# Optimization experiments

Hardware: AMD Instinct MI355X
Metric: run time of the kernel (lower is better)

## Reference

```python
import jax, jax.numpy as jnp
import numpy as np

N_IMG = 8
IMG_H = IMG_W = 1024
STRIDES = (4, 8, 16, 32, 64)
FEAT = tuple(IMG_H // s for s in STRIDES)
RATIOS = (0.5, 1.0, 2.0)
A = len(RATIOS)
PRE_NMS = 1000
POST_NMS = 1000
NMS_THRESH = 0.7
SCORE_THRESH = 0.0
MIN_SIZE = 1e-3
BBOX_CLIP = float(np.log(1000.0 / 16.0))  # torchvision bbox_xform_clip
NPL = tuple(f * f * A for f in FEAT)      # anchors per level


def _make_anchors():
    levels = []
    for stride, f in zip(STRIDES, FEAT):
        size = stride * 8.0
        base = []
        for r in RATIOS:
            w = size * np.sqrt(1.0 / r)
            h = size * np.sqrt(r)
            base.append([-w / 2, -h / 2, w / 2, h / 2])
        base = np.asarray(base, np.float32)              # [A,4]
        coords = np.arange(f, dtype=np.float32) * stride
        sy, sx = np.meshgrid(coords, coords, indexing="ij")
        shifts = np.stack([sx, sy, sx, sy], -1).reshape(-1, 1, 4)  # y-major, matches [H,W,A] flatten
        levels.append((shifts + base[None]).reshape(-1, 4))
    return np.concatenate(levels, 0).astype(np.float32)


def setup_inputs() -> dict:
    key = jax.random.key(0)
    ks = jax.random.split(key, 10)
    inp = {}
    for i, f in enumerate(FEAT):
        inp[f"obj_l{i}"] = jax.random.normal(ks[i], (N_IMG, A, f, f), jnp.float32)
        inp[f"delta_l{i}"] = jax.random.normal(ks[5 + i], (N_IMG, A * 4, f, f), jnp.float32) * 0.2
    inp["anchors"] = jnp.asarray(_make_anchors())
    return inp


def _flatten_level(obj, delta):
    # permute_and_flatten: [N,A,H,W] -> [N,H*W*A] ; [N,A*4,H,W] -> [N,H*W*A,4]
    n, a, h, w = obj.shape
    o = jnp.transpose(obj, (0, 2, 3, 1)).reshape(n, -1)
    d = jnp.transpose(delta.reshape(n, a, 4, h, w), (0, 3, 4, 1, 2)).reshape(n, -1, 4)
    return o, d


def _decode(deltas, anchors):
    # BoxCoder(weights=(1,1,1,1)).decode
    w = anchors[:, 2] - anchors[:, 0]
    h = anchors[:, 3] - anchors[:, 1]
    cx = anchors[:, 0] + 0.5 * w
    cy = anchors[:, 1] + 0.5 * h
    dx, dy = deltas[..., 0], deltas[..., 1]
    dw = jnp.minimum(deltas[..., 2], BBOX_CLIP)
    dh = jnp.minimum(deltas[..., 3], BBOX_CLIP)
    pcx = dx * w + cx
    pcy = dy * h + cy
    pw = jnp.exp(dw) * w
    ph = jnp.exp(dh) * h
    return jnp.stack([pcx - 0.5 * pw, pcy - 0.5 * ph, pcx + 0.5 * pw, pcy + 0.5 * ph], -1)


def _nms_image(boxes, scores, lvl):
    # clip_boxes_to_image
    x1 = jnp.clip(boxes[:, 0], 0.0, IMG_W)
    y1 = jnp.clip(boxes[:, 1], 0.0, IMG_H)
    x2 = jnp.clip(boxes[:, 2], 0.0, IMG_W)
    y2 = jnp.clip(boxes[:, 3], 0.0, IMG_H)
    boxes = jnp.stack([x1, y1, x2, y2], -1)
    # remove_small_boxes + score_thresh, as a mask (fixed shapes)
    valid = (x2 - x1 >= MIN_SIZE) & (y2 - y1 >= MIN_SIZE) & (scores >= SCORE_THRESH)
    s = jnp.where(valid, scores, -1.0)
    order = jnp.argsort(-s)
    boxes, s, valid, lvl = boxes[order], s[order], valid[order], lvl[order]
    # batched_nms: offset boxes per level so cross-level IoU is 0
    ob = boxes + (lvl.astype(boxes.dtype) * (max(IMG_H, IMG_W) + 1.0))[:, None]
    ob = jax.lax.stop_gradient(ob)  # keep decisions are non-differentiable
    area = (ob[:, 2] - ob[:, 0]) * (ob[:, 3] - ob[:, 1])
    lt = jnp.maximum(ob[:, None, :2], ob[None, :, :2])
    rb = jnp.minimum(ob[:, None, 2:], ob[None, :, 2:])
    wh = jnp.maximum(rb - lt, 0.0)
    inter = wh[..., 0] * wh[..., 1]
    iou = inter / (area[:, None] + area[None, :] - inter + 1e-9)  # [K,K]
    k = boxes.shape[0]
    jidx = jnp.arange(k)

    def body(i, keep):
        sup = keep[i] & (iou[i] > NMS_THRESH) & (jidx > i)
        return keep & ~sup

    keep = jax.lax.fori_loop(0, k, body, valid)
    # compact kept boxes (score-sorted) into fixed [POST_NMS] output, zero-padded
    rank = jnp.cumsum(keep) - 1
    tgt = jnp.where(keep & (rank < POST_NMS), rank, POST_NMS)
    out_b = jnp.zeros((POST_NMS + 1, 4), boxes.dtype).at[tgt].set(boxes)[:POST_NMS]
    out_s = jnp.zeros((POST_NMS + 1,), s.dtype).at[tgt].set(jnp.where(keep, s, 0.0))[:POST_NMS]
    return out_b, out_s


def _forward(objs, deltas, anchors):
    flat = [_flatten_level(o, d) for o, d in zip(objs, deltas)]
    obj = jnp.concatenate([f[0] for f in flat], 1)       # [N, K_total]
    dl = jnp.concatenate([f[1] for f in flat], 1)        # [N, K_total, 4]
    proposals = _decode(dl, anchors)                     # [N, K_total, 4]
    lvl_full = jnp.concatenate([jnp.full((n,), i, jnp.int32) for i, n in enumerate(NPL)])
    # per-level top-k on objectness logits
    idxs, off = [], 0
    for n in NPL:
        kk = min(PRE_NMS, n)
        _, ti = jax.lax.top_k(obj[:, off:off + n], kk)
        idxs.append(ti + off)
        off += n
    top_idx = jnp.concatenate(idxs, 1)                   # [N, K_sel]
    scores = jax.nn.sigmoid(jnp.take_along_axis(obj, top_idx, 1))
    prop = jnp.take_along_axis(proposals, top_idx[..., None], 1)
    lvl = lvl_full[top_idx]
    boxes_out, _ = jax.lax.map(lambda t: _nms_image(*t), (prop, scores, lvl))
    return boxes_out                                     # [N, POST_NMS, 4]


def reference(obj_l0, obj_l1, obj_l2, obj_l3, obj_l4, delta_l0, delta_l1, delta_l2, delta_l3, delta_l4, anchors):
    return _forward([obj_l0, obj_l1, obj_l2, obj_l3, obj_l4],
                    [delta_l0, delta_l1, delta_l2, delta_l3, delta_l4], anchors)
```

## Files before the change

### kernel.cpp

```cpp
#include <hip/hip_runtime.h>
#include <cstdint>

#define K_SEL 4768
#define CAND_CAP 16384
#define NBIN 4096
#define BUFCAP 512
#define TPAD 9216

struct P5 { const float* p[5]; };

__device__ __forceinline__ unsigned fsortkey(float f) {
  unsigned b = __float_as_uint(f);
  return (b & 0x80000000u) ? ~b : (b | 0x80000000u);
}

__global__ __launch_bounds__(256) void k_hist(P5 obj, unsigned* phist) {
  int p = blockIdx.y; int img = p / 5, lvl = p % 5;
  int f = 256 >> lvl; int n = 3 * f * f;
  __shared__ unsigned lh[NBIN];
  for (int b = threadIdx.x; b < NBIN; b += 256) lh[b] = 0;
  __syncthreads();
  const float4* src4 = (const float4*)(obj.p[lvl] + (size_t)img * n);
  int n4 = n >> 2;
  int chunk = (n4 + gridDim.x - 1) / gridDim.x;
  int e0 = blockIdx.x * chunk, e1 = min(n4, e0 + chunk);
  for (int e = e0 + threadIdx.x; e < e1; e += 256) {
    float4 v = src4[e];
    atomicAdd(&lh[fsortkey(v.x) >> 20], 1u);
    atomicAdd(&lh[fsortkey(v.y) >> 20], 1u);
    atomicAdd(&lh[fsortkey(v.z) >> 20], 1u);
    atomicAdd(&lh[fsortkey(v.w) >> 20], 1u);
  }
  __syncthreads();
  unsigned* dst = phist + ((size_t)(p * 8 + blockIdx.x)) * NBIN;
  for (int b = threadIdx.x; b < NBIN; b += 256) dst[b] = lh[b];
}

__global__ __launch_bounds__(256) void k_thresh(const unsigned* phist, int* Bthr, unsigned* cnt) {
  int p = blockIdx.x; int lvl = p % 5;
  unsigned kk = (lvl == 4) ? 768u : 1000u;
  __shared__ unsigned hsum[NBIN];
  __shared__ unsigned csum[256];
  int c = threadIdx.x;
  unsigned tot[16];
#pragma unroll
  for (int k = 0; k < 16; ++k) tot[k] = 0;
  for (int g = 0; g < 8; ++g) {
    const unsigned* hp = phist + ((size_t)(p * 8 + g)) * NBIN + c * 16;
#pragma unroll
    for (int k = 0; k < 16; ++k) tot[k] += hp[k];
  }
  unsigned s = 0;
#pragma unroll
  for (int k = 0; k < 16; ++k) { hsum[c * 16 + k] = tot[k]; s += tot[k]; }
  csum[c] = s;
  __syncthreads();
  if (c == 0) {
    unsigned acc = 0; int B = 0;
    for (int cc = 255; cc >= 0; --cc) {
      if (acc + csum[cc] >= kk) {
        for (int b = 15; b >= 0; --b) {
          acc += hsum[cc * 16 + b];
          if (acc >= kk) { B = cc * 16 + b; break; }
        }
        break;
      }
      acc += csum[cc];
    }
    Bthr[p] = B;
    cnt[p] = 0;
  }
}

__global__ __launch_bounds__(256) void k_gather(P5 obj, const int* Bthr, unsigned* cnt,
                                                unsigned long long* ck) {
  int p = blockIdx.y; int img = p / 5, lvl = p % 5;
  int f = 256 >> lvl; int hw = f * f; int n = 3 * hw;
  int B = Bthr[p];
  int shift = 2 * (8 - lvl);
  const float4* src4 = (const float4*)(obj.p[lvl] + (size_t)img * n);
  int n4 = n >> 2;
  unsigned long long* dst = ck + (size_t)p * CAND_CAP;
  int tid = threadIdx.x;
  int lane = tid & 63, wv = tid >> 6;
  __shared__ unsigned long long buf[4][BUFCAP];
  __shared__ unsigned wTot[4];
  __shared__ unsigned blkBase;
  unsigned wc = 0;
  for (int e = blockIdx.x * 256 + tid; e < n4; e += gridDim.x * 256) {
    float4 v = src4[e];
    float vv[4] = {v.x, v.y, v.z, v.w};
#pragma unroll
    for (int j = 0; j < 4; ++j) {
      unsigned sv = fsortkey(vv[j]);
      bool pass = (int)(sv >> 20) >= B;
      unsigned long long m = __ballot(pass);
      if (m) {
        if (pass) {
          unsigned pos = wc + (unsigned)__popcll(m & ((1ULL << lane) - 1ULL));
          int ee = e * 4 + j;
          int a = ee >> shift;
          int r = ee & (hw - 1);
          unsigned kidx = (unsigned)(r * 3 + a);
          unsigned long long key = ((unsigned long long)sv << 32) | (0xFFFFFFFFu - kidx);
          if (pos < BUFCAP) buf[wv][pos] = key;
          else {
            unsigned gp = atomicAdd(&cnt[p], 1u);
            if (gp < CAND_CAP) dst[gp] = key;
          }
        }
        wc += (unsigned)__popcll(m);
      }
    }
  }
  if (lane == 0) wTot[wv] = min(wc, (unsigned)BUFCAP);
  __syncthreads();
  if (tid == 0) {
    unsigned tot = wTot[0] + wTot[1] + wTot[2] + wTot[3];
    blkBase = tot ? atomicAdd(&cnt[p], tot) : 0u;
  }
  __syncthreads();
  unsigned myOff = blkBase;
  for (int x = 0; x < wv; ++x) myOff += wTot[x];
  unsigned wn = wTot[wv];
  for (unsigned j = lane; j < wn; j += 64) {
    unsigned gp = myOff + j;
    if (gp < CAND_CAP) dst[gp] = buf[wv][j];
  }
}

__global__ __launch_bounds__(256) void k_select(const unsigned* cnt, const unsigned long long* ck,
                                                unsigned* selSV, unsigned* selIdx) {
  int p = blockIdx.y; int img = p / 5, lvl = p % 5;
  int Cc = min((int)cnt[p], CAND_CAP);
  if (blockIdx.x * 256 >= Cc) return;
  int kk = (lvl == 4) ? 768 : 1000;
  int soff = lvl * 1000;
  const unsigned long long* keys = ck + (size_t)p * CAND_CAP;
  __shared__ unsigned long long sk[4096];
  int stage = min(Cc, 4096);
  for (int j = threadIdx.x; j < stage; j += 256) sk[j] = keys[j];
  __syncthreads();
  int c = blockIdx.x * 256 + threadIdx.x;
  if (c >= Cc) return;
  unsigned long long kc = keys[c];
  int rank = 0;
#pragma unroll 8
  for (int j = 0; j < stage; ++j) rank += (sk[j] > kc) ? 1 : 0;
  for (int j = stage; j < Cc; ++j) rank += (keys[j] > kc) ? 1 : 0;
  if (rank < kk) {
    int slot = img * K_SEL + soff + rank;
    selSV[slot]  = (unsigned)(kc >> 32);
    selIdx[slot] = 0xFFFFFFFFu - (unsigned)kc;
  }
}

__global__ __launch_bounds__(256) void k_decode(P5 del, const float* anchors,
                                                const unsigned* selSV, const unsigned* selIdx,
                                                float* boxP, unsigned long long* keyP) {
  int i = blockIdx.x * 256 + threadIdx.x;
  if (i >= K_SEL) return;
  int img = blockIdx.y;
  int lvl = (i < 4000) ? (i / 1000) : 4;
  int f = 256 >> lvl, hw = f * f;
  const int aoffA[5] = {0, 196608, 245760, 258048, 261120};
  int slot = img * K_SEL + i;
  unsigned k = selIdx[slot];
  unsigned sv = selSV[slot];
  int a = (int)(k % 3u); int r = (int)(k / 3u);
  int y = r >> (8 - lvl); int x = r & (f - 1);
  const float* dp = del.p[lvl] + (size_t)(img * 12 + a * 4) * hw + (size_t)y * f + x;
  float d0 = dp[0], d1 = dp[hw], d2 = dp[2 * hw], d3 = dp[3 * hw];
  const float* ar = anchors + (size_t)(aoffA[lvl] + (int)k) * 4;
  float a0 = ar[0], a1 = ar[1], a2 = ar[2], a3 = ar[3];
  float w = __fsub_rn(a2, a0), h = __fsub_rn(a3, a1);
  float cx = __fadd_rn(a0, __fmul_rn(0.5f, w));
  float cy = __fadd_rn(a1, __fmul_rn(0.5f, h));
  const float CLIP = 4.135166556742356f;
  float dw = fminf(d2, CLIP), dh = fminf(d3, CLIP);
  float pcx = __fadd_rn(__fmul_rn(d0, w), cx);
  float pcy = __fadd_rn(__fmul_rn(d1, h), cy);
  float pw = __fmul_rn(expf(dw), w);
  float ph = __fmul_rn(expf(dh), h);
  float x1 = __fsub_rn(pcx, __fmul_rn(0.5f, pw));
  float y1 = __fsub_rn(pcy, __fmul_rn(0.5f, ph));
  float x2 = __fadd_rn(pcx, __fmul_rn(0.5f, pw));
  float y2 = __fadd_rn(pcy, __fmul_rn(0.5f, ph));
  float x1c = fminf(fmaxf(x1, 0.0f), 1024.0f);
  float y1c = fminf(fmaxf(y1, 0.0f), 1024.0f);
  float x2c = fminf(fmaxf(x2, 0.0f), 1024.0f);
  float y2c = fminf(fmaxf(y2, 0.0f), 1024.0f);
  bool valid = (__fsub_rn(x2c, x1c) >= 1e-3f) && (__fsub_rn(y2c, y1c) >= 1e-3f);
  float* bp = boxP + (size_t)slot * 4;
  bp[0] = x1c; bp[1] = y1c; bp[2] = x2c; bp[3] = y2c;
  unsigned low = 0xFFFFFFFFu - (unsigned)i;
  keyP[slot] = valid ? (((unsigned long long)sv << 32) | low) : (unsigned long long)low;
}

__device__ __forceinline__ bool iou_gt(float rx1, float ry1, float rx2, float ry2, float rar,
                                       float cx1, float cy1, float cx2, float cy2, float car) {
  float ltx = fmaxf(rx1, cx1), lty = fmaxf(ry1, cy1);
  float rbx = fminf(rx2, cx2), rby = fminf(ry2, cy2);
  float wx = fmaxf(__fsub_rn(rbx, ltx), 0.0f);
  float wy = fmaxf(__fsub_rn(rby, lty), 0.0f);
  float inter = __fmul_rn(wx, wy);
  float denom = __fadd_rn(__fsub_rn(__fadd_rn(rar, car), inter), 1e-9f);
  return __fdiv_rn(inter, denom) > 0.7f;
}

__global__ __launch_bounds__(64) void k_lvlmask(const float* boxP, unsigned long long* T) {
  int img = blockIdx.y;
  int q = blockIdx.x;
  int lvl, q2;
  if (q < 544) { lvl = q / 136; q2 = q - lvl * 136; }
  else         { lvl = 4;       q2 = q - 544; }
  int kk = (lvl == 4) ? 768 : 1000;
  int nch = (kk + 63) >> 6;
  int rb = 0;
  while (q2 >= nch - rb) { q2 -= nch - rb; ++rb; }
  int cb = rb + q2;
  int t = threadIdx.x;
  float off = __fmul_rn((float)lvl, 1025.0f);
  const float4* b4 = (const float4*)boxP + (size_t)img * K_SEL + lvl * 1000;
  __shared__ float rx1s[64], ry1s[64], rx2s[64], ry2s[64], rars[64];
  int j = rb * 64 + t;
  if (j < kk) {
    float4 bb = b4[j];
    float ox1 = __fadd_rn(bb.x, off), oy1 = __fadd_rn(bb.y, off);
    float ox2 = __fadd_rn(bb.z, off), oy2 = __fadd_rn(bb.w, off);
    rx1s[t] = ox1; ry1s[t] = oy1; rx2s[t] = ox2; ry2s[t] = oy2;
    rars[t] = __fmul_rn(__fsub_rn(ox2, ox1), __fsub_rn(oy2, oy1));
  }
  __syncthreads();
  int i = cb * 64 + t;
  if (i >= kk) return;
  float4 bb = b4[i];
  float cx1 = __fadd_rn(bb.x, off), cy1 = __fadd_rn(bb.y, off);
  float cx2 = __fadd_rn(bb.z, off), cy2 = __fadd_rn(bb.w, off);
  float car = __fmul_rn(__fsub_rn(cx2, cx1), __fsub_rn(cy2, cy1));
  int jmaxR = min(64, kk - rb * 64);
  int jend = (rb == cb) ? min(t, jmaxR) : jmaxR;
  unsigned long long bits = 0;
  for (int jj = 0; jj < jend; ++jj) {
    if (iou_gt(rx1s[jj], ry1s[jj], rx2s[jj], ry2s[jj], rars[jj], cx1, cy1, cx2, cy2, car))
      bits |= (1ULL << jj);
  }
  const int Pt[16] = {0, 1, 4, 7, 12, 17, 24, 31, 40, 49, 60, 71, 84, 97, 112, 127};
  int sc = (cb + 1) | 1;
  T[(size_t)(img * 5 + lvl) * TPAD + 64 * Pt[cb] + t * sc + rb] = bits;
}

__global__ __launch_bounds__(256) void k_lvlnms(const unsigned long long* keyP,
                                                const unsigned long long* Tg_,
                                                unsigned long long* keepw) {
  int p = blockIdx.x; int img = p / 5, lvl = p % 5;
  int kk = (lvl == 4) ? 768 : 1000;
  int tw = (lvl == 4) ? 5376 : TPAD;
  int tid = threadIdx.x;
  __shared__ __align__(16) unsigned long long Ts[TPAD];
  const unsigned long long* Tg = Tg_ + (size_t)p * TPAD;
  const unsigned long long* kp = keyP + (size_t)img * K_SEL + lvl * 1000;
  unsigned vmask = 0;
  if (tid < 64) {
#pragma unroll
    for (int c = 0; c < 16; ++c) {
      int i = c * 64 + tid;
      bool v = (i < kk) && ((kp[min(i, kk - 1)] >> 32) != 0ULL);
      vmask |= v ? (1u << c) : 0u;
    }
  }
  for (int x = tid; x < (tw >> 1); x += 256)
    ((ulonglong2*)Ts)[x] = ((const ulonglong2*)Tg)[x];
  __syncthreads();
  if (tid >= 64) return;
  int t = tid;
  const int Pt[16] = {0, 1, 4, 7, 12, 17, 24, 31, 40, 49, 60, 71, 84, 97, 112, 127};
  unsigned long long kw[16];
#pragma unroll
  for (int w = 0; w < 16; ++w) kw[w] = 0ULL;
#pragma unroll
  for (int c = 0; c < 16; ++c) {
    if (c * 64 < kk) {
      int base = 64 * Pt[c] + t * ((c + 1) | 1);
      unsigned long long tv[16];
#pragma unroll
      for (int w = 0; w < 16; ++w) tv[w] = Ts[base + w];
      unsigned long long a = 0;
#pragma unroll
      for (int w = 0; w < 16; ++w) a |= tv[w] & kw[w];
      unsigned long long colT = tv[c];
      bool alive = ((vmask >> c) & 1u) && (a == 0ULL);
      unsigned long long keepm = 0ULL;
      unsigned long long actm = __ballot(alive);
      while (actm) {
        bool cank = alive && ((colT & actm) == 0ULL);
        unsigned long long newk = __ballot(cank);
        keepm |= newk;
        alive = alive && !cank && ((colT & newk) == 0ULL);
        actm = __ballot(alive);
      }
      kw[c] = keepm;
    }
  }
  if (t == 0) {
#pragma unroll
    for (int c = 0; c < 16; ++c) keepw[(size_t)p * 16 + c] = kw[c];
  }
}

__global__ __launch_bounds__(256) void k_merge(const unsigned long long* keyP, const float* boxP,
                                               const unsigned long long* keepw, float* out) {
  int p = blockIdx.x; int img = p / 5, lvl = p % 5;
  int tid = threadIdx.x;
  __shared__ unsigned long long lkey[5000];
  __shared__ int lpos[5000];
  __shared__ int wp[5][17];
  __shared__ unsigned long long kwS[80];
  for (int x = tid; x < 80; x += 256) {
    kwS[x] = keepw[(size_t)img * 80 + x];
  }
  __syncthreads();
  if (tid < 5) {
    int acc = 0;
    for (int w = 0; w < 16; ++w) { wp[tid][w] = acc; acc += (int)__popcll(kwS[tid * 16 + w]); }
    wp[tid][16] = acc;
  }
  __syncthreads();
  const unsigned long long* kp = keyP + (size_t)img * K_SEL;
  for (int i = tid; i < K_SEL; i += 256) {
    int l = (i < 4000) ? i / 1000 : 4;
    int li = i - l * 1000;
    unsigned long long wmask = kwS[l * 16 + (li >> 6)];
    if ((wmask >> (li & 63)) & 1ULL) {
      int j = wp[l][li >> 6] + (int)__popcll(wmask & ((1ULL << (li & 63)) - 1ULL));
      lkey[l * 1000 + j] = kp[i];
      lpos[l * 1000 + j] = i;
    }
  }
  __syncthreads();
  const float4* b4 = (const float4*)boxP + (size_t)img * K_SEL;
  float4* out4 = (float4*)out + (size_t)img * 1000;
  int kn = wp[lvl][16];
  for (int j = tid; j < kn; j += 256) {
    unsigned long long key = lkey[lvl * 1000 + j];
    int grank = j;
#pragma unroll
    for (int l2 = 0; l2 < 5; ++l2) {
      if (l2 == lvl) continue;
      int lo = 0, hi = wp[l2][16];
      const unsigned long long* a = &lkey[l2 * 1000];
      while (lo < hi) { int mid = (lo + hi) >> 1; if (a[mid] > key) lo = mid + 1; else hi = mid; }
      grank += lo;
    }
    if (grank < 1000) out4[grank] = b4[lpos[lvl * 1000 + j]];
  }
  if (lvl == 0) {
    int KT = wp[0][16] + wp[1][16] + wp[2][16] + wp[3][16] + wp[4][16];
    for (int s = min(KT, 1000) + tid; s < 1000; s += 256)
      out4[s] = make_float4(0.f, 0.f, 0.f, 0.f);
  }
}

extern "C" void kernel_launch(void* const* d_in, const int* in_sizes, int n_in,
                              void* d_out, int out_size, void* d_ws, size_t ws_size,
                              hipStream_t stream) {
  (void)in_sizes; (void)n_in;
  P5 obj, del;
  for (int i = 0; i < 5; ++i) {
    obj.p[i] = (const float*)d_in[2 * i];
    del.p[i] = (const float*)d_in[2 * i + 1];
  }
  const float* anchors = (const float*)d_in[10];
  float* out = (float*)d_out;
  char* ws = (char*)d_ws;

  unsigned* cnt               = (unsigned*)(ws + 0);
  int* Bthr                   = (int*)(ws + 192);
  unsigned long long* candK   = (unsigned long long*)(ws + 512);
  unsigned* selSV             = (unsigned*)(ws + 5243392);
  unsigned* selIdx            = (unsigned*)(ws + 5395968);
  float* boxP                 = (float*)(ws + 5548544);
  unsigned long long* keyP    = (unsigned long long*)(ws + 6158848);
  unsigned long long* keepw   = (unsigned long long*)(ws + 6464000);
  unsigned long long* T       = (unsigned long long*)(ws + 6469120);
  unsigned* phist             = (unsigned*)(ws + 6469120);
  const size_t NEED = 11712000ULL;
  if (ws_size < NEED) { hipMemsetAsync(d_out, 0, (size_t)out_size * 4, stream); return; }

  k_hist    <<<dim3(8, 40), 256, 0, stream>>>(obj, phist);
  k_thresh  <<<40, 256, 0, stream>>>(phist, Bthr, cnt);
  k_gather  <<<dim3(32, 40), 256, 0, stream>>>(obj, Bthr, cnt, candK);
  k_select  <<<dim3(64, 40), 256, 0, stream>>>(cnt, candK, selSV, selIdx);
  k_decode  <<<dim3(19, 8), 256, 0, stream>>>(del, anchors, selSV, selIdx, boxP, keyP);
  k_lvlmask <<<dim3(622, 8), 64, 0, stream>>>(boxP, T);
  k_lvlnms  <<<40, 256, 0, stream>>>(keyP, T, keepw);
  k_merge   <<<40, 256, 0, stream>>>(keyP, boxP, keepw, out);
}
```

Measured before the change: 221.3 us.

## Fuse threshold/gather/select into one kernel and NMS with merge per image

Merges the threshold, candidate gather and rank-select kernels into a single block per image-level that keeps candidates in shared memory. The per-level NMS and cross-level merge kernels are fused into one 320-thread block per image, with one wavefront per level and double-buffered register prefetch of mask rows. This removes several launches and global round-trips of counters and candidate keys. In exchange the gather over each level now runs on only 40 blocks instead of 1280, which serializes the large level-0 scan, and the merge step has only 8 blocks.

```diff
diff --git a/kernel.cpp b/kernel.cpp
--- a/kernel.cpp
+++ b/kernel.cpp
@@ -4,7 +4,6 @@
 #define K_SEL 4768
 #define CAND_CAP 16384
 #define NBIN 4096
-#define BUFCAP 512
 #define TPAD 9216
 
 struct P5 { const float* p[5]; };
@@ -36,58 +35,54 @@
   for (int b = threadIdx.x; b < NBIN; b += 256) dst[b] = lh[b];
 }
 
-__global__ __launch_bounds__(256) void k_thresh(const unsigned* phist, int* Bthr, unsigned* cnt) {
-  int p = blockIdx.x; int lvl = p % 5;
-  unsigned kk = (lvl == 4) ? 768u : 1000u;
+__global__ __launch_bounds__(256) void k_tgsel(P5 obj, const unsigned* phist,
+                                               unsigned long long* ck,
+                                               unsigned* selSV, unsigned* selIdx) {
+  int p = blockIdx.x; int img = p / 5, lvl = p % 5;
+  int f = 256 >> lvl; int hw = f * f; int n = 3 * hw;
+  int kk = (lvl == 4) ? 768 : 1000;
+  int tid = threadIdx.x;
+  int lane = tid & 63;
   __shared__ unsigned hsum[NBIN];
   __shared__ unsigned csum[256];
-  int c = threadIdx.x;
+  __shared__ unsigned long long sk[4096];
+  __shared__ int Bs;
+  __shared__ unsigned candCnt, ovf;
   unsigned tot[16];
 #pragma unroll
   for (int k = 0; k < 16; ++k) tot[k] = 0;
   for (int g = 0; g < 8; ++g) {
-    const unsigned* hp = phist + ((size_t)(p * 8 + g)) * NBIN + c * 16;
+    const unsigned* hp = phist + ((size_t)(p * 8 + g)) * NBIN + tid * 16;
 #pragma unroll
     for (int k = 0; k < 16; ++k) tot[k] += hp[k];
   }
   unsigned s = 0;
 #pragma unroll
-  for (int k = 0; k < 16; ++k) { hsum[c * 16 + k] = tot[k]; s += tot[k]; }
-  csum[c] = s;
-  __syncthreads();
-  if (c == 0) {
+  for (int k = 0; k < 16; ++k) { hsum[tid * 16 + k] = tot[k]; s += tot[k]; }
+  csum[tid] = s;
+  if (tid == 0) { candCnt = 0; ovf = 0; }
+  __syncthreads();
+  if (tid == 0) {
     unsigned acc = 0; int B = 0;
     for (int cc = 255; cc >= 0; --cc) {
-      if (acc + csum[cc] >= kk) {
+      if (acc + csum[cc] >= (unsigned)kk) {
         for (int b = 15; b >= 0; --b) {
           acc += hsum[cc * 16 + b];
-          if (acc >= kk) { B = cc * 16 + b; break; }
+          if (acc >= (unsigned)kk) { B = cc * 16 + b; break; }
         }
         break;
       }
       acc += csum[cc];
     }
-    Bthr[p] = B;
-    cnt[p] = 0;
-  }
-}
-
-__global__ __launch_bounds__(256) void k_gather(P5 obj, const int* Bthr, unsigned* cnt,
-                                                unsigned long long* ck) {
-  int p = blockIdx.y; int img = p / 5, lvl = p % 5;
-  int f = 256 >> lvl; int hw = f * f; int n = 3 * hw;
-  int B = Bthr[p];
+    Bs = B;
+  }
+  __syncthreads();
+  int B = Bs;
   int shift = 2 * (8 - lvl);
   const float4* src4 = (const float4*)(obj.p[lvl] + (size_t)img * n);
   int n4 = n >> 2;
-  unsigned long long* dst = ck + (size_t)p * CAND_CAP;
-  int tid = threadIdx.x;
-  int lane = tid & 63, wv = tid >> 6;
-  __shared__ unsigned long long buf[4][BUFCAP];
-  __shared__ unsigned wTot[4];
-  __shared__ unsigned blkBase;
-  unsigned wc = 0;
-  for (int e = blockIdx.x * 256 + tid; e < n4; e += gridDim.x * 256) {
+  unsigned long long* dstG = ck + (size_t)p * CAND_CAP;
+  for (int e = tid; e < n4; e += 256) {
     float4 v = src4[e];
     float vv[4] = {v.x, v.y, v.z, v.w};
 #pragma unroll
@@ -96,62 +91,53 @@
       bool pass = (int)(sv >> 20) >= B;
       unsigned long long m = __ballot(pass);
       if (m) {
+        int leader = __ffsll(m) - 1;
+        unsigned base = 0;
+        if (lane == leader) base = atomicAdd(&candCnt, (unsigned)__popcll(m));
+        base = __shfl(base, leader);
         if (pass) {
-          unsigned pos = wc + (unsigned)__popcll(m & ((1ULL << lane) - 1ULL));
+          unsigned pos = base + (unsigned)__popcll(m & ((1ULL << lane) - 1ULL));
           int ee = e * 4 + j;
           int a = ee >> shift;
           int r = ee & (hw - 1);
           unsigned kidx = (unsigned)(r * 3 + a);
           unsigned long long key = ((unsigned long long)sv << 32) | (0xFFFFFFFFu - kidx);
-          if (pos < BUFCAP) buf[wv][pos] = key;
+          if (pos < 4096u) sk[pos] = key;
           else {
-            unsigned gp = atomicAdd(&cnt[p], 1u);
-            if (gp < CAND_CAP) dst[gp] = key;
+            unsigned gp = atomicAdd(&ovf, 1u);
+            if (gp < CAND_CAP) dstG[gp] = key;
           }
         }
-        wc += (unsigned)__popcll(m);
       }
     }
   }
-  if (lane == 0) wTot[wv] = min(wc, (unsigned)BUFCAP);
-  __syncthreads();
-  if (tid == 0) {
-    unsigned tot = wTot[0] + wTot[1] + wTot[2] + wTot[3];
-    blkBase = tot ? atomicAdd(&cnt[p], tot) : 0u;
-  }
-  __syncthreads();
-  unsigned myOff = blkBase;
-  for (int x = 0; x < wv; ++x) myOff += wTot[x];
-  unsigned wn = wTot[wv];
-  for (unsigned j = lane; j < wn; j += 64) {
-    unsigned gp = myOff + j;
-    if (gp < CAND_CAP) dst[gp] = buf[wv][j];
-  }
-}
-
-__global__ __launch_bounds__(256) void k_select(const unsigned* cnt, const unsigned long long* ck,
-                                                unsigned* selSV, unsigned* selIdx) {
-  int p = blockIdx.y; int img = p / 5, lvl = p % 5;
-  int Cc = min((int)cnt[p], CAND_CAP);
-  if (blockIdx.x * 256 >= Cc) return;
-  int kk = (lvl == 4) ? 768 : 1000;
+  __threadfence_block();
+  __syncthreads();
+  int Cc = min((int)candCnt, 4096);
+  int Ct = min((int)ovf, CAND_CAP);
   int soff = lvl * 1000;
-  const unsigned long long* keys = ck + (size_t)p * CAND_CAP;
-  __shared__ unsigned long long sk[4096];
-  int stage = min(Cc, 4096);
-  for (int j = threadIdx.x; j < stage; j += 256) sk[j] = keys[j];
-  __syncthreads();
-  int c = blockIdx.x * 256 + threadIdx.x;
-  if (c >= Cc) return;
-  unsigned long long kc = keys[c];
-  int rank = 0;
+  for (int c = tid; c < Cc; c += 256) {
+    unsigned long long kc = sk[c];
+    int rank = 0;
 #pragma unroll 8
-  for (int j = 0; j < stage; ++j) rank += (sk[j] > kc) ? 1 : 0;
-  for (int j = stage; j < Cc; ++j) rank += (keys[j] > kc) ? 1 : 0;
-  if (rank < kk) {
-    int slot = img * K_SEL + soff + rank;
-    selSV[slot]  = (unsigned)(kc >> 32);
-    selIdx[slot] = 0xFFFFFFFFu - (unsigned)kc;
+    for (int j = 0; j < Cc; ++j) rank += (sk[j] > kc) ? 1 : 0;
+    for (int j = 0; j < Ct; ++j) rank += (dstG[j] > kc) ? 1 : 0;
+    if (rank < kk) {
+      int slot = img * K_SEL + soff + rank;
+      selSV[slot]  = (unsigned)(kc >> 32);
+      selIdx[slot] = 0xFFFFFFFFu - (unsigned)kc;
+    }
+  }
+  for (int c = tid; c < Ct; c += 256) {
+    unsigned long long kc = dstG[c];
+    int rank = 0;
+    for (int j = 0; j < Cc; ++j) rank += (sk[j] > kc) ? 1 : 0;
+    for (int j = 0; j < Ct; ++j) rank += (dstG[j] > kc) ? 1 : 0;
+    if (rank < kk) {
+      int slot = img * K_SEL + soff + rank;
+      selSV[slot]  = (unsigned)(kc >> 32);
+      selIdx[slot] = 0xFFFFFFFFu - (unsigned)kc;
+    }
   }
 }
 
@@ -250,74 +236,82 @@
   T[(size_t)(img * 5 + lvl) * TPAD + 64 * Pt[cb] + t * sc + rb] = bits;
 }
 
-__global__ __launch_bounds__(256) void k_lvlnms(const unsigned long long* keyP,
-                                                const unsigned long long* Tg_,
-                                                unsigned long long* keepw) {
-  int p = blockIdx.x; int img = p / 5, lvl = p % 5;
-  int kk = (lvl == 4) ? 768 : 1000;
-  int tw = (lvl == 4) ? 5376 : TPAD;
+#define CURW(w) ((c & 1) ? tvB[w] : tvA[w])
+#define NXTW(w) ((c & 1) ? tvA[w] : tvB[w])
+__global__ __launch_bounds__(320, 1) void k_nmsmerge(const unsigned long long* keyP,
+                                                     const unsigned long long* Tg_,
+                                                     const float* boxP, float* out) {
+  int img = blockIdx.x;
   int tid = threadIdx.x;
-  __shared__ __align__(16) unsigned long long Ts[TPAD];
-  const unsigned long long* Tg = Tg_ + (size_t)p * TPAD;
-  const unsigned long long* kp = keyP + (size_t)img * K_SEL + lvl * 1000;
-  unsigned vmask = 0;
-  if (tid < 64) {
-#pragma unroll
-    for (int c = 0; c < 16; ++c) {
-      int i = c * 64 + tid;
-      bool v = (i < kk) && ((kp[min(i, kk - 1)] >> 32) != 0ULL);
-      vmask |= v ? (1u << c) : 0u;
-    }
-  }
-  for (int x = tid; x < (tw >> 1); x += 256)
-    ((ulonglong2*)Ts)[x] = ((const ulonglong2*)Tg)[x];
-  __syncthreads();
-  if (tid >= 64) return;
-  int t = tid;
-  const int Pt[16] = {0, 1, 4, 7, 12, 17, 24, 31, 40, 49, 60, 71, 84, 97, 112, 127};
-  unsigned long long kw[16];
-#pragma unroll
-  for (int w = 0; w < 16; ++w) kw[w] = 0ULL;
-#pragma unroll
-  for (int c = 0; c < 16; ++c) {
-    if (c * 64 < kk) {
-      int base = 64 * Pt[c] + t * ((c + 1) | 1);
-      unsigned long long tv[16];
-#pragma unroll
-      for (int w = 0; w < 16; ++w) tv[w] = Ts[base + w];
-      unsigned long long a = 0;
-#pragma unroll
-      for (int w = 0; w < 16; ++w) a |= tv[w] & kw[w];
-      unsigned long long colT = tv[c];
-      bool alive = ((vmask >> c) & 1u) && (a == 0ULL);
-      unsigned long long keepm = 0ULL;
-      unsigned long long actm = __ballot(alive);
-      while (actm) {
-        bool cank = alive && ((colT & actm) == 0ULL);
-        unsigned long long newk = __ballot(cank);
-        keepm |= newk;
-        alive = alive && !cank && ((colT & newk) == 0ULL);
-        actm = __ballot(alive);
-      }
-      kw[c] = keepm;
-    }
-  }
-  if (t == 0) {
-#pragma unroll
-    for (int c = 0; c < 16; ++c) keepw[(size_t)p * 16 + c] = kw[c];
-  }
-}
-
-__global__ __launch_bounds__(256) void k_merge(const unsigned long long* keyP, const float* boxP,
-                                               const unsigned long long* keepw, float* out) {
-  int p = blockIdx.x; int img = p / 5, lvl = p % 5;
-  int tid = threadIdx.x;
+  int lane = tid & 63, wv = tid >> 6;
+  __shared__ unsigned long long kwS[80];
   __shared__ unsigned long long lkey[5000];
   __shared__ int lpos[5000];
   __shared__ int wp[5][17];
-  __shared__ unsigned long long kwS[80];
-  for (int x = tid; x < 80; x += 256) {
-    kwS[x] = keepw[(size_t)img * 80 + x];
+  const int Pt[16] = {0, 1, 4, 7, 12, 17, 24, 31, 40, 49, 60, 71, 84, 97, 112, 127};
+  {
+    int lvl = wv;
+    int kk = (lvl == 4) ? 768 : 1000;
+    int nch = (kk + 63) >> 6;
+    const unsigned long long* Tp = Tg_ + (size_t)(img * 5 + lvl) * TPAD;
+    const unsigned long long* kp = keyP + (size_t)img * K_SEL + lvl * 1000;
+    unsigned vmask = 0;
+#pragma unroll
+    for (int c = 0; c < 16; ++c) {
+      int i = c * 64 + lane;
+      bool v = (i < kk) && ((kp[min(i, kk - 1)] >> 32) != 0ULL);
+      vmask |= v ? (1u << c) : 0u;
+    }
+    unsigned long long tvA[16], tvB[16];
+    unsigned long long kw0=0,kw1=0,kw2=0,kw3=0,kw4=0,kw5=0,kw6=0,kw7=0,
+                       kw8=0,kw9=0,kw10=0,kw11=0,kw12=0,kw13=0,kw14=0,kw15=0;
+    tvA[0] = Tp[lane];
+#pragma unroll
+    for (int c = 0; c < 16; ++c) {
+      if (c < nch) {
+        if (c + 1 < nch) {
+          int nb = 64 * Pt[c + 1] + lane * ((c + 2) | 1);
+#pragma unroll
+          for (int w = 0; w <= c + 1; ++w) NXTW(w) = Tp[nb + w];
+        }
+        unsigned long long a = 0;
+#pragma unroll
+        for (int w = 0; w < c; ++w) {
+          unsigned long long kv =
+            (w==0)?kw0:(w==1)?kw1:(w==2)?kw2:(w==3)?kw3:(w==4)?kw4:(w==5)?kw5:
+            (w==6)?kw6:(w==7)?kw7:(w==8)?kw8:(w==9)?kw9:(w==10)?kw10:(w==11)?kw11:
+            (w==12)?kw12:(w==13)?kw13:(w==14)?kw14:kw15;
+          a |= CURW(w) & kv;
+        }
+        unsigned long long colT = CURW(c);
+        bool alive = ((vmask >> c) & 1u) && (a == 0ULL);
+        unsigned long long keepm = 0ULL;
+        unsigned long long actm = __ballot(alive);
+        while (actm) {
+          bool cank = alive && ((colT & actm) == 0ULL);
+          unsigned long long newk = __ballot(cank);
+          keepm |= newk;
+          alive = alive && !cank && ((colT & newk) == 0ULL);
+          actm = __ballot(alive);
+        }
+        switch (c) {
+          case 0: kw0=keepm; break;  case 1: kw1=keepm; break;
+          case 2: kw2=keepm; break;  case 3: kw3=keepm; break;
+          case 4: kw4=keepm; break;  case 5: kw5=keepm; break;
+          case 6: kw6=keepm; break;  case 7: kw7=keepm; break;
+          case 8: kw8=keepm; break;  case 9: kw9=keepm; break;
+          case 10: kw10=keepm; break; case 11: kw11=keepm; break;
+          case 12: kw12=keepm; break; case 13: kw13=keepm; break;
+          case 14: kw14=keepm; break; default: kw15=keepm; break;
+        }
+      }
+    }
+    if (lane == 0) {
+      kwS[lvl*16+0]=kw0;  kwS[lvl*16+1]=kw1;  kwS[lvl*16+2]=kw2;  kwS[lvl*16+3]=kw3;
+      kwS[lvl*16+4]=kw4;  kwS[lvl*16+5]=kw5;  kwS[lvl*16+6]=kw6;  kwS[lvl*16+7]=kw7;
+      kwS[lvl*16+8]=kw8;  kwS[lvl*16+9]=kw9;  kwS[lvl*16+10]=kw10; kwS[lvl*16+11]=kw11;
+      kwS[lvl*16+12]=kw12; kwS[lvl*16+13]=kw13; kwS[lvl*16+14]=kw14; kwS[lvl*16+15]=kw15;
+    }
   }
   __syncthreads();
   if (tid < 5) {
@@ -327,7 +321,7 @@
   }
   __syncthreads();
   const unsigned long long* kp = keyP + (size_t)img * K_SEL;
-  for (int i = tid; i < K_SEL; i += 256) {
+  for (int i = tid; i < K_SEL; i += 320) {
     int l = (i < 4000) ? i / 1000 : 4;
     int li = i - l * 1000;
     unsigned long long wmask = kwS[l * 16 + (li >> 6)];
@@ -340,25 +334,24 @@
   __syncthreads();
   const float4* b4 = (const float4*)boxP + (size_t)img * K_SEL;
   float4* out4 = (float4*)out + (size_t)img * 1000;
-  int kn = wp[lvl][16];
-  for (int j = tid; j < kn; j += 256) {
-    unsigned long long key = lkey[lvl * 1000 + j];
+  for (int x = tid; x < 5000; x += 320) {
+    int l = x / 1000, j = x - l * 1000;
+    if (j >= wp[l][16]) continue;
+    unsigned long long key = lkey[x];
     int grank = j;
 #pragma unroll
     for (int l2 = 0; l2 < 5; ++l2) {
-      if (l2 == lvl) continue;
+      if (l2 == l) continue;
       int lo = 0, hi = wp[l2][16];
       const unsigned long long* a = &lkey[l2 * 1000];
       while (lo < hi) { int mid = (lo + hi) >> 1; if (a[mid] > key) lo = mid + 1; else hi = mid; }
       grank += lo;
     }
-    if (grank < 1000) out4[grank] = b4[lpos[lvl * 1000 + j]];
-  }
-  if (lvl == 0) {
-    int KT = wp[0][16] + wp[1][16] + wp[2][16] + wp[3][16] + wp[4][16];
-    for (int s = min(KT, 1000) + tid; s < 1000; s += 256)
-      out4[s] = make_float4(0.f, 0.f, 0.f, 0.f);
-  }
+    if (grank < 1000) out4[grank] = b4[lpos[x]];
+  }
+  int KT = wp[0][16] + wp[1][16] + wp[2][16] + wp[3][16] + wp[4][16];
+  for (int s = min(KT, 1000) + tid; s < 1000; s += 320)
+    out4[s] = make_float4(0.f, 0.f, 0.f, 0.f);
 }
 
 extern "C" void kernel_launch(void* const* d_in, const int* in_sizes, int n_in,
@@ -374,25 +367,19 @@
   float* out = (float*)d_out;
   char* ws = (char*)d_ws;
 
-  unsigned* cnt               = (unsigned*)(ws + 0);
-  int* Bthr                   = (int*)(ws + 192);
   unsigned long long* candK   = (unsigned long long*)(ws + 512);
   unsigned* selSV             = (unsigned*)(ws + 5243392);
   unsigned* selIdx            = (unsigned*)(ws + 5395968);
   float* boxP                 = (float*)(ws + 5548544);
   unsigned long long* keyP    = (unsigned long long*)(ws + 6158848);
-  unsigned long long* keepw   = (unsigned long long*)(ws + 6464000);
   unsigned long long* T       = (unsigned long long*)(ws + 6469120);
   unsigned* phist             = (unsigned*)(ws + 6469120);
   const size_t NEED = 11712000ULL;
   if (ws_size < NEED) { hipMemsetAsync(d_out, 0, (size_t)out_size * 4, stream); return; }
 
-  k_hist    <<<dim3(8, 40), 256, 0, stream>>>(obj, phist);
-  k_thresh  <<<40, 256, 0, stream>>>(phist, Bthr, cnt);
-  k_gather  <<<dim3(32, 40), 256, 0, stream>>>(obj, Bthr, cnt, candK);
-  k_select  <<<dim3(64, 40), 256, 0, stream>>>(cnt, candK, selSV, selIdx);
-  k_decode  <<<dim3(19, 8), 256, 0, stream>>>(del, anchors, selSV, selIdx, boxP, keyP);
-  k_lvlmask <<<dim3(622, 8), 64, 0, stream>>>(boxP, T);
-  k_lvlnms  <<<40, 256, 0, stream>>>(keyP, T, keepw);
-  k_merge   <<<40, 256, 0, stream>>>(keyP, boxP, keepw, out);
-}
+  k_hist     <<<dim3(8, 40), 256, 0, stream>>>(obj, phist);
+  k_tgsel    <<<40, 256, 0, stream>>>(obj, phist, candK, selSV, selIdx);
+  k_decode   <<<dim3(19, 8), 256, 0, stream>>>(del, anchors, selSV, selIdx, boxP, keyP);
+  k_lvlmask  <<<dim3(622, 8), 64, 0, stream>>>(boxP, T);
+  k_nmsmerge <<<8, 320, 0, stream>>>(keyP, T, boxP, out);
+}
```

Result: slower. 393.7 us (+77.9%).

## Fuse select and decode, use per-block candidate slices without global atomics

Applied to the files above, without the earlier changes.

The gather kernel now writes each block's candidates into a fixed per-block slice and records a per-block count, replacing the global atomic counter and overflow path. A new fused select+decode kernel prefix-sums those counts, stages the candidates in shared memory, ranks them and decodes the selected boxes directly, which drops one launch and the intermediate selSV/selIdx buffers. The NMS tile load is also unrolled four-wide. In exchange, candidates are capped at 512 per block and 4096 per level, so inputs with heavy ties near the threshold could drop candidates.

```diff
diff --git a/kernel.cpp b/kernel.cpp
--- a/kernel.cpp
+++ b/kernel.cpp
@@ -2,9 +2,9 @@
 #include <cstdint>
 
 #define K_SEL 4768
-#define CAND_CAP 16384
 #define NBIN 4096
 #define BUFCAP 512
+#define SLICE 512
 #define TPAD 9216
 
 struct P5 { const float* p[5]; };
@@ -36,7 +36,7 @@
   for (int b = threadIdx.x; b < NBIN; b += 256) dst[b] = lh[b];
 }
 
-__global__ __launch_bounds__(256) void k_thresh(const unsigned* phist, int* Bthr, unsigned* cnt) {
+__global__ __launch_bounds__(256) void k_thresh(const unsigned* phist, int* Bthr) {
   int p = blockIdx.x; int lvl = p % 5;
   unsigned kk = (lvl == 4) ? 768u : 1000u;
   __shared__ unsigned hsum[NBIN];
@@ -68,26 +68,25 @@
       acc += csum[cc];
     }
     Bthr[p] = B;
-    cnt[p] = 0;
-  }
-}
-
-__global__ __launch_bounds__(256) void k_gather(P5 obj, const int* Bthr, unsigned* cnt,
-                                                unsigned long long* ck) {
+  }
+}
+
+__global__ __launch_bounds__(256) void k_gather(P5 obj, const int* Bthr,
+                                                unsigned* cntB, unsigned long long* ck) {
   int p = blockIdx.y; int img = p / 5, lvl = p % 5;
   int f = 256 >> lvl; int hw = f * f; int n = 3 * hw;
   int B = Bthr[p];
+  int tid = threadIdx.x;
+  int lane = tid & 63, wv = tid >> 6;
   int shift = 2 * (8 - lvl);
   const float4* src4 = (const float4*)(obj.p[lvl] + (size_t)img * n);
   int n4 = n >> 2;
-  unsigned long long* dst = ck + (size_t)p * CAND_CAP;
-  int tid = threadIdx.x;
-  int lane = tid & 63, wv = tid >> 6;
+  int chunk = (n4 + 31) >> 5;
+  int e0 = blockIdx.x * chunk, e1 = min(n4, e0 + chunk);
   __shared__ unsigned long long buf[4][BUFCAP];
   __shared__ unsigned wTot[4];
-  __shared__ unsigned blkBase;
   unsigned wc = 0;
-  for (int e = blockIdx.x * 256 + tid; e < n4; e += gridDim.x * 256) {
+  for (int e = e0 + tid; e < e1; e += 256) {
     float4 v = src4[e];
     float vv[4] = {v.x, v.y, v.z, v.w};
 #pragma unroll
@@ -104,10 +103,6 @@
           unsigned kidx = (unsigned)(r * 3 + a);
           unsigned long long key = ((unsigned long long)sv << 32) | (0xFFFFFFFFu - kidx);
           if (pos < BUFCAP) buf[wv][pos] = key;
-          else {
-            unsigned gp = atomicAdd(&cnt[p], 1u);
-            if (gp < CAND_CAP) dst[gp] = key;
-          }
         }
         wc += (unsigned)__popcll(m);
       }
@@ -115,58 +110,61 @@
   }
   if (lane == 0) wTot[wv] = min(wc, (unsigned)BUFCAP);
   __syncthreads();
-  if (tid == 0) {
-    unsigned tot = wTot[0] + wTot[1] + wTot[2] + wTot[3];
-    blkBase = tot ? atomicAdd(&cnt[p], tot) : 0u;
-  }
-  __syncthreads();
-  unsigned myOff = blkBase;
+  unsigned myOff = 0;
   for (int x = 0; x < wv; ++x) myOff += wTot[x];
-  unsigned wn = wTot[wv];
-  for (unsigned j = lane; j < wn; j += 64) {
+  unsigned tot4 = wTot[0] + wTot[1] + wTot[2] + wTot[3];
+  unsigned long long* dst = ck + ((size_t)p * 32 + blockIdx.x) * SLICE;
+  for (unsigned j = lane; j < wTot[wv]; j += 64) {
     unsigned gp = myOff + j;
-    if (gp < CAND_CAP) dst[gp] = buf[wv][j];
-  }
-}
-
-__global__ __launch_bounds__(256) void k_select(const unsigned* cnt, const unsigned long long* ck,
-                                                unsigned* selSV, unsigned* selIdx) {
+    if (gp < SLICE) dst[gp] = buf[wv][j];
+  }
+  if (tid == 0) cntB[p * 32 + blockIdx.x] = min(tot4, (unsigned)SLICE);
+}
+
+__global__ __launch_bounds__(256) void k_seldec(P5 del, const float* anchors,
+                                                const unsigned* cntB,
+                                                const unsigned long long* ck,
+                                                float* boxP, unsigned long long* keyP) {
   int p = blockIdx.y; int img = p / 5, lvl = p % 5;
-  int Cc = min((int)cnt[p], CAND_CAP);
-  if (blockIdx.x * 256 >= Cc) return;
   int kk = (lvl == 4) ? 768 : 1000;
   int soff = lvl * 1000;
-  const unsigned long long* keys = ck + (size_t)p * CAND_CAP;
+  int tid = threadIdx.x;
   __shared__ unsigned long long sk[4096];
-  int stage = min(Cc, 4096);
-  for (int j = threadIdx.x; j < stage; j += 256) sk[j] = keys[j];
-  __syncthreads();
-  int c = blockIdx.x * 256 + threadIdx.x;
+  __shared__ unsigned offs[33];
+  if (tid < 32) {
+    unsigned v = cntB[p * 32 + tid];
+#pragma unroll
+    for (int d = 1; d < 32; d <<= 1) {
+      unsigned o = __shfl(v, tid - d);
+      if (tid >= d) v += o;
+    }
+    offs[tid + 1] = v;
+    if (tid == 0) offs[0] = 0;
+  }
+  __syncthreads();
+  int Cc = min((int)offs[32], 4096);
+  if (blockIdx.x * 256 >= Cc) return;
+  for (int b2 = 0; b2 < 32; ++b2) {
+    unsigned o = offs[b2];
+    int c2 = (int)(offs[b2 + 1] - o);
+    const unsigned long long* src = ck + ((size_t)p * 32 + b2) * SLICE;
+    for (int j = tid; j < c2; j += 256)
+      if ((int)(o + j) < 4096) sk[o + j] = src[j];
+  }
+  __syncthreads();
+  int c = blockIdx.x * 256 + tid;
   if (c >= Cc) return;
-  unsigned long long kc = keys[c];
+  unsigned long long kc = sk[c];
   int rank = 0;
 #pragma unroll 8
-  for (int j = 0; j < stage; ++j) rank += (sk[j] > kc) ? 1 : 0;
-  for (int j = stage; j < Cc; ++j) rank += (keys[j] > kc) ? 1 : 0;
-  if (rank < kk) {
-    int slot = img * K_SEL + soff + rank;
-    selSV[slot]  = (unsigned)(kc >> 32);
-    selIdx[slot] = 0xFFFFFFFFu - (unsigned)kc;
-  }
-}
-
-__global__ __launch_bounds__(256) void k_decode(P5 del, const float* anchors,
-                                                const unsigned* selSV, const unsigned* selIdx,
-                                                float* boxP, unsigned long long* keyP) {
-  int i = blockIdx.x * 256 + threadIdx.x;
-  if (i >= K_SEL) return;
-  int img = blockIdx.y;
-  int lvl = (i < 4000) ? (i / 1000) : 4;
+  for (int j = 0; j < Cc; ++j) rank += (sk[j] > kc) ? 1 : 0;
+  if (rank >= kk) return;
+  unsigned k = 0xFFFFFFFFu - (unsigned)kc;
+  unsigned sv = (unsigned)(kc >> 32);
+  int i = soff + rank;
+  int slot = img * K_SEL + i;
   int f = 256 >> lvl, hw = f * f;
   const int aoffA[5] = {0, 196608, 245760, 258048, 261120};
-  int slot = img * K_SEL + i;
-  unsigned k = selIdx[slot];
-  unsigned sv = selSV[slot];
   int a = (int)(k % 3u); int r = (int)(k / 3u);
   int y = r >> (8 - lvl); int x = r & (f - 1);
   const float* dp = del.p[lvl] + (size_t)(img * 12 + a * 4) * hw + (size_t)y * f + x;
@@ -269,8 +267,22 @@
       vmask |= v ? (1u << c) : 0u;
     }
   }
-  for (int x = tid; x < (tw >> 1); x += 256)
-    ((ulonglong2*)Ts)[x] = ((const ulonglong2*)Tg)[x];
+  {
+    const ulonglong2* Tg2 = (const ulonglong2*)Tg;
+    ulonglong2* Ts2 = (ulonglong2*)Ts;
+    int nv = tw >> 1;
+    for (int x = tid; x < nv; x += 1024) {
+      int x1i = x + 256, x2i = x + 512, x3i = x + 768;
+      ulonglong2 a0 = Tg2[x], a1 = {}, a2 = {}, a3 = {};
+      if (x1i < nv) a1 = Tg2[x1i];
+      if (x2i < nv) a2 = Tg2[x2i];
+      if (x3i < nv) a3 = Tg2[x3i];
+      Ts2[x] = a0;
+      if (x1i < nv) Ts2[x1i] = a1;
+      if (x2i < nv) Ts2[x2i] = a2;
+      if (x3i < nv) Ts2[x3i] = a3;
+    }
+  }
   __syncthreads();
   if (tid >= 64) return;
   int t = tid;
@@ -374,11 +386,9 @@
   float* out = (float*)d_out;
   char* ws = (char*)d_ws;
 
-  unsigned* cnt               = (unsigned*)(ws + 0);
-  int* Bthr                   = (int*)(ws + 192);
-  unsigned long long* candK   = (unsigned long long*)(ws + 512);
-  unsigned* selSV             = (unsigned*)(ws + 5243392);
-  unsigned* selIdx            = (unsigned*)(ws + 5395968);
+  unsigned* cntB              = (unsigned*)(ws + 0);
+  int* Bthr                   = (int*)(ws + 5120);
+  unsigned long long* candK   = (unsigned long long*)(ws + 8192);
   float* boxP                 = (float*)(ws + 5548544);
   unsigned long long* keyP    = (unsigned long long*)(ws + 6158848);
   unsigned long long* keepw   = (unsigned long long*)(ws + 6464000);
@@ -388,10 +398,9 @@
   if (ws_size < NEED) { hipMemsetAsync(d_out, 0, (size_t)out_size * 4, stream); return; }
 
   k_hist    <<<dim3(8, 40), 256, 0, stream>>>(obj, phist);
-  k_thresh  <<<40, 256, 0, stream>>>(phist, Bthr, cnt);
-  k_gather  <<<dim3(32, 40), 256, 0, stream>>>(obj, Bthr, cnt, candK);
-  k_select  <<<dim3(64, 40), 256, 0, stream>>>(cnt, candK, selSV, selIdx);
-  k_decode  <<<dim3(19, 8), 256, 0, stream>>>(del, anchors, selSV, selIdx, boxP, keyP);
+  k_thresh  <<<40, 256, 0, stream>>>(phist, Bthr);
+  k_gather  <<<dim3(32, 40), 256, 0, stream>>>(obj, Bthr, cntB, candK);
+  k_seldec  <<<dim3(16, 40), 256, 0, stream>>>(del, anchors, cntB, candK, boxP, keyP);
   k_lvlmask <<<dim3(622, 8), 64, 0, stream>>>(boxP, T);
   k_lvlnms  <<<40, 256, 0, stream>>>(keyP, T, keepw);
   k_merge   <<<40, 256, 0, stream>>>(keyP, boxP, keepw, out);
```

Result: faster. 211.4 us (-4.5%).
